# Kernel tuning notes

Measured on AMD Instinct MI355X. Metric: run time of the kernel, lower is better.

The kernel has to match this reference:

```python
import jax, jax.numpy as jnp
import numpy as np

IN_C, OUT_C, HEADS = 128, 64, 2
N_USER, N_ITEM, E = 100000, 50000, 500000
NEG_SLOPE = 0.2


def _params(key, in_c, out_c, heads):
    ks = jax.random.split(key, 4)
    s_lin = 1.0 / np.sqrt(in_c)
    s_att = 1.0 / np.sqrt(out_c)
    return dict(
        Wl=jax.random.normal(ks[0], (in_c, heads * out_c), jnp.float32) * s_lin,
        bl=jnp.zeros((heads * out_c,), jnp.float32),
        Wr=jax.random.normal(ks[1], (in_c, heads * out_c), jnp.float32) * s_lin,
        br=jnp.zeros((heads * out_c,), jnp.float32),
        att=jax.random.normal(ks[2], (heads, out_c), jnp.float32) * s_att,
        bias=jnp.zeros((out_c,), jnp.float32),
    )


def setup_inputs() -> dict:
    key = jax.random.key(0)
    k = jax.random.split(key, 8)
    inp = {
        "x_user": jax.random.normal(k[0], (N_USER, IN_C), jnp.float32),
        "x_item": jax.random.normal(k[1], (N_ITEM, IN_C), jnp.float32),
        "src_u2i": jax.random.randint(k[2], (E,), 0, N_USER, jnp.int32),
        "dst_u2i": jax.random.randint(k[3], (E,), 0, N_ITEM, jnp.int32),
        "src_i2u": jax.random.randint(k[4], (E,), 0, N_ITEM, jnp.int32),
        "dst_i2u": jax.random.randint(k[5], (E,), 0, N_USER, jnp.int32),
    }
    p_u2i = _params(k[6], IN_C, OUT_C, HEADS)
    p_i2u = _params(k[7], IN_C, OUT_C, HEADS)
    for n, v in p_u2i.items():
        inp[n + "_u2i"] = v
    for n, v in p_i2u.items():
        inp[n + "_i2u"] = v
    return inp


def gatv2_conv(x_src, x_dst, src, dst, Wl, bl, Wr, br, att, bias, n_dst):
    # lin_l on source nodes, lin_r on destination nodes -> [N, H, C]
    xl = (x_src @ Wl + bl).reshape(-1, HEADS, OUT_C)
    xr = (x_dst @ Wr + br).reshape(-1, HEADS, OUT_C)
    xj = xl[src]  # [E, H, C] gathered source features
    xi = xr[dst]  # [E, H, C] gathered dest features
    e = jax.nn.leaky_relu(xi + xj, NEG_SLOPE)
    logits = jnp.einsum("ehc,hc->eh", e, att)  # [E, H]
    # numerically stable segment softmax over incoming edges per dest node
    m = jax.ops.segment_max(logits, dst, num_segments=n_dst)
    m = jnp.where(jnp.isfinite(m), m, 0.0)  # guard empty segments
    a = jnp.exp(logits - m[dst])
    denom = jax.ops.segment_sum(a, dst, num_segments=n_dst)
    alpha = a / (denom[dst] + 1e-16)
    out = jax.ops.segment_sum(alpha[:, :, None] * xj, dst, num_segments=n_dst)
    return out.mean(axis=1) + bias  # concat=False -> head mean, then bias


def reference(x_user, x_item, src_u2i, dst_u2i, src_i2u, dst_i2u,
              Wl_u2i, bl_u2i, Wr_u2i, br_u2i, att_u2i, bias_u2i,
              Wl_i2u, bl_i2u, Wr_i2u, br_i2u, att_i2u, bias_i2u):
    # HeteroConv with aggr='sum': one edge type per destination node type here
    out_item = gatv2_conv(x_user, x_item, src_u2i, dst_u2i,
                          Wl_u2i, bl_u2i, Wr_u2i, br_u2i, att_u2i, bias_u2i, N_ITEM)
    out_user = gatv2_conv(x_item, x_user, src_i2u, dst_i2u,
                          Wl_i2u, bl_i2u, Wr_i2u, br_i2u, att_i2u, bias_i2u, N_USER)
    return out_user, out_item
```

## Files before the change

### kernel.cpp

```cpp
#include <hip/hip_runtime.h>

#define SCAN_B 1024

__global__ __launch_bounds__(256) void k_zero(int* __restrict__ cnt, int n) {
    int i = blockIdx.x * 256 + threadIdx.x;
    if (i < n) cnt[i] = 0;
}

__global__ __launch_bounds__(256) void k_hist(
    const int* __restrict__ dst_a, const int* __restrict__ dst_b,
    int* __restrict__ cnt, int n_a, int E)
{
    int i = blockIdx.x * 256 + threadIdx.x;
    if (i >= 2 * E) return;
    int idx = (i < E) ? dst_a[i] : (n_a + dst_b[i - E]);
    atomicAdd(&cnt[idx], 1);
}

__global__ __launch_bounds__(SCAN_B) void k_scan1(
    const int* __restrict__ cnt, int n, int* __restrict__ rowptr, int* __restrict__ bsum)
{
    __shared__ int tmp[SCAN_B];
    int i = blockIdx.x * SCAN_B + threadIdx.x;
    int v = (i < n) ? cnt[i] : 0;
    tmp[threadIdx.x] = v;
    __syncthreads();
    for (int off = 1; off < SCAN_B; off <<= 1) {
        int t = (threadIdx.x >= (unsigned)off) ? tmp[threadIdx.x - off] : 0;
        __syncthreads();
        tmp[threadIdx.x] += t;
        __syncthreads();
    }
    if (i < n) rowptr[i] = tmp[threadIdx.x] - v;
    if (threadIdx.x == SCAN_B - 1) bsum[blockIdx.x] = tmp[threadIdx.x];
}

__global__ __launch_bounds__(SCAN_B) void k_scan2(int* __restrict__ bsum, int nb) {
    __shared__ int tmp[SCAN_B];
    int i = threadIdx.x;
    int v = (i < nb) ? bsum[i] : 0;
    tmp[i] = v;
    __syncthreads();
    for (int off = 1; off < SCAN_B; off <<= 1) {
        int t = (i >= off) ? tmp[i - off] : 0;
        __syncthreads();
        tmp[i] += t;
        __syncthreads();
    }
    if (i < nb) bsum[i] = tmp[i] - v;
}

__global__ __launch_bounds__(256) void k_scan3(
    int* __restrict__ rowptr, int* __restrict__ cursor,
    const int* __restrict__ bsum, int n, int total)
{
    int i = blockIdx.x * 256 + threadIdx.x;
    if (i < n) {
        int r = rowptr[i] + bsum[i / SCAN_B];
        rowptr[i] = r;
        cursor[i] = r;
    }
    if (i == 0) rowptr[n] = total;
}

__global__ __launch_bounds__(256) void k_fill(
    const int* __restrict__ src_a, const int* __restrict__ dst_a,
    const int* __restrict__ src_b, const int* __restrict__ dst_b,
    int* __restrict__ cursor, int* __restrict__ sorted_src, int n_a, int E)
{
    int i = blockIdx.x * 256 + threadIdx.x;
    if (i >= 2 * E) return;
    int idx, s;
    if (i < E) { idx = dst_a[i];            s = src_a[i]; }
    else       { idx = n_a + dst_b[i - E];  s = src_b[i - E]; }
    int pos = atomicAdd(&cursor[idx], 1);
    sorted_src[pos] = s;
}

__global__ __launch_bounds__(256) void gemm128x2(
    const float* __restrict__ X0,
    const float* __restrict__ W00, const float* __restrict__ B00, float* __restrict__ Y00,
    const float* __restrict__ W01, const float* __restrict__ B01, float* __restrict__ Y01,
    int M0, int nb0,
    const float* __restrict__ X1,
    const float* __restrict__ W10, const float* __restrict__ B10, float* __restrict__ Y10,
    const float* __restrict__ W11, const float* __restrict__ B11, float* __restrict__ Y11,
    int M1)
{
    __shared__ float xs[64][20];
    __shared__ float ws[16][256];

    const float *X, *W0, *B0, *W1, *B1;
    float *Y0, *Y1;
    int M, bid;
    if ((int)blockIdx.x < nb0) {
        X = X0; W0 = W00; B0 = B00; Y0 = Y00; W1 = W01; B1 = B01; Y1 = Y01;
        M = M0; bid = blockIdx.x;
    } else {
        X = X1; W0 = W10; B0 = B10; Y0 = Y10; W1 = W11; B1 = B11; Y1 = Y11;
        M = M1; bid = blockIdx.x - nb0;
    }

    const int tid = threadIdx.x;
    const int m0  = bid * 64;
    const int r0  = (tid >> 4) * 4;
    const int c0  = (tid & 15) * 4;

    float acc[4][16];
#pragma unroll
    for (int i = 0; i < 4; ++i)
#pragma unroll
        for (int j = 0; j < 16; ++j) acc[i][j] = 0.0f;

    for (int kc = 0; kc < 128; kc += 16) {
        {
            int row = tid >> 2;
            int kq  = (tid & 3) * 4;
            float4 v = make_float4(0.f, 0.f, 0.f, 0.f);
            if (m0 + row < M)
                v = *(const float4*)&X[(size_t)(m0 + row) * 128 + kc + kq];
            *(float4*)&xs[row][kq] = v;
        }
#pragma unroll
        for (int i = 0; i < 4; ++i) {
            int f = tid + i * 256;
            int k = f >> 6;
            int q = (f & 63) * 4;
            float4 v = (q < 128)
                ? *(const float4*)&W0[(size_t)(kc + k) * 128 + q]
                : *(const float4*)&W1[(size_t)(kc + k) * 128 + (q - 128)];
            *(float4*)&ws[k][q] = v;
        }
        __syncthreads();

#pragma unroll
        for (int k = 0; k < 16; k += 4) {
            float4 a0 = *(const float4*)&xs[r0 + 0][k];
            float4 a1 = *(const float4*)&xs[r0 + 1][k];
            float4 a2 = *(const float4*)&xs[r0 + 2][k];
            float4 a3 = *(const float4*)&xs[r0 + 3][k];
#pragma unroll
            for (int kk = 0; kk < 4; ++kk) {
                float4 b0 = *(const float4*)&ws[k + kk][c0];
                float4 b1 = *(const float4*)&ws[k + kk][c0 + 64];
                float4 b2 = *(const float4*)&ws[k + kk][c0 + 128];
                float4 b3 = *(const float4*)&ws[k + kk][c0 + 192];
                float av[4] = { ((const float*)&a0)[kk], ((const float*)&a1)[kk],
                                ((const float*)&a2)[kk], ((const float*)&a3)[kk] };
#pragma unroll
                for (int i = 0; i < 4; ++i) {
                    float a = av[i];
                    acc[i][0]  += a * b0.x; acc[i][1]  += a * b0.y;
                    acc[i][2]  += a * b0.z; acc[i][3]  += a * b0.w;
                    acc[i][4]  += a * b1.x; acc[i][5]  += a * b1.y;
                    acc[i][6]  += a * b1.z; acc[i][7]  += a * b1.w;
                    acc[i][8]  += a * b2.x; acc[i][9]  += a * b2.y;
                    acc[i][10] += a * b2.z; acc[i][11] += a * b2.w;
                    acc[i][12] += a * b3.x; acc[i][13] += a * b3.y;
                    acc[i][14] += a * b3.z; acc[i][15] += a * b3.w;
                }
            }
        }
        __syncthreads();
    }

    float4 p00 = *(const float4*)&B0[c0];
    float4 p01 = *(const float4*)&B0[c0 + 64];
    float4 p10 = *(const float4*)&B1[c0];
    float4 p11 = *(const float4*)&B1[c0 + 64];
#pragma unroll
    for (int i = 0; i < 4; ++i) {
        int row = m0 + r0 + i;
        if (row < M) {
            *(float4*)&Y0[(size_t)row * 128 + c0] = make_float4(
                acc[i][0] + p00.x, acc[i][1] + p00.y, acc[i][2] + p00.z, acc[i][3] + p00.w);
            *(float4*)&Y0[(size_t)row * 128 + c0 + 64] = make_float4(
                acc[i][4] + p01.x, acc[i][5] + p01.y, acc[i][6] + p01.z, acc[i][7] + p01.w);
            *(float4*)&Y1[(size_t)row * 128 + c0] = make_float4(
                acc[i][8] + p10.x, acc[i][9] + p10.y, acc[i][10] + p10.z, acc[i][11] + p10.w);
            *(float4*)&Y1[(size_t)row * 128 + c0 + 64] = make_float4(
                acc[i][12] + p11.x, acc[i][13] + p11.y, acc[i][14] + p11.z, acc[i][15] + p11.w);
        }
    }
}

__global__ __launch_bounds__(256) void k_gat2(
    const float* __restrict__ xl_a, const float* __restrict__ xr_a,
    const float* __restrict__ att_a, const float* __restrict__ bias_a,
    float* __restrict__ out_a,
    const float* __restrict__ xl_b, const float* __restrict__ xr_b,
    const float* __restrict__ att_b, const float* __restrict__ bias_b,
    float* __restrict__ out_b,
    const int* __restrict__ rowptr, const int* __restrict__ srcs,
    int n_a, int n_all)
{
    int wave = (blockIdx.x * 256 + threadIdx.x) >> 6;
    if (wave >= n_all) return;
    const int lane = threadIdx.x & 63;
    const int h = lane >> 5;
    const int j = lane & 31;
    const int ch = h * 64 + 2 * j;

    const float *xl, *xr, *att, *bias;
    float* out;
    int d;
    if (wave < n_a) { xl = xl_a; xr = xr_a; att = att_a; bias = bias_a; out = out_a; d = wave; }
    else            { xl = xl_b; xr = xr_b; att = att_b; bias = bias_b; out = out_b; d = wave - n_a; }

    const int base = rowptr[wave];
    const int end  = rowptr[wave + 1];
    if (base == end) {
        if (lane < 32) {
            float2 bv = *(const float2*)&bias[2 * j];
            *(float2*)&out[(size_t)d * 64 + 2 * j] = bv;
        }
        return;
    }

    const float2 xi = *(const float2*)&xr[(size_t)d * 128 + ch];
    const float2 at = *(const float2*)&att[ch];

    float den = 0.f, a0 = 0.f, a1 = 0.f;
    int k = base;
    for (; k + 1 < end; k += 2) {
        int s0 = srcs[k];
        int s1 = srcs[k + 1];
        float2 x0 = *(const float2*)&xl[(size_t)s0 * 128 + ch];
        float2 x1 = *(const float2*)&xl[(size_t)s1 * 128 + ch];
        float e00 = xi.x + x0.x, e01 = xi.y + x0.y;
        float e10 = xi.x + x1.x, e11 = xi.y + x1.y;
        e00 = fmaxf(e00, 0.2f * e00);
        e01 = fmaxf(e01, 0.2f * e01);
        e10 = fmaxf(e10, 0.2f * e10);
        e11 = fmaxf(e11, 0.2f * e11);
        float p0 = e00 * at.x + e01 * at.y;
        float p1 = e10 * at.x + e11 * at.y;
        p0 += __shfl_xor(p0, 1, 64);  p1 += __shfl_xor(p1, 1, 64);
        p0 += __shfl_xor(p0, 2, 64);  p1 += __shfl_xor(p1, 2, 64);
        p0 += __shfl_xor(p0, 4, 64);  p1 += __shfl_xor(p1, 4, 64);
        p0 += __shfl_xor(p0, 8, 64);  p1 += __shfl_xor(p1, 8, 64);
        p0 += __shfl_xor(p0, 16, 64); p1 += __shfl_xor(p1, 16, 64);
        float w0 = __expf(p0);
        float w1 = __expf(p1);
        den += w0 + w1;
        a0  += w0 * x0.x + w1 * x1.x;
        a1  += w0 * x0.y + w1 * x1.y;
    }
    if (k < end) {
        int s0 = srcs[k];
        float2 x0 = *(const float2*)&xl[(size_t)s0 * 128 + ch];
        float e00 = xi.x + x0.x, e01 = xi.y + x0.y;
        e00 = fmaxf(e00, 0.2f * e00);
        e01 = fmaxf(e01, 0.2f * e01);
        float p0 = e00 * at.x + e01 * at.y;
        p0 += __shfl_xor(p0, 1, 64);
        p0 += __shfl_xor(p0, 2, 64);
        p0 += __shfl_xor(p0, 4, 64);
        p0 += __shfl_xor(p0, 8, 64);
        p0 += __shfl_xor(p0, 16, 64);
        float w0 = __expf(p0);
        den += w0;
        a0  += w0 * x0.x;
        a1  += w0 * x0.y;
    }

    float inv = 1.0f / (den + 1e-16f);
    float r0 = a0 * inv;
    float r1 = a1 * inv;
    float q0 = __shfl_xor(r0, 32, 64);
    float q1 = __shfl_xor(r1, 32, 64);
    if (lane < 32) {
        float2 bv = *(const float2*)&bias[2 * j];
        float2 o = make_float2(0.5f * (r0 + q0) + bv.x,
                               0.5f * (r1 + q1) + bv.y);
        *(float2*)&out[(size_t)d * 64 + 2 * j] = o;
    }
}

extern "C" void kernel_launch(void* const* d_in, const int* in_sizes, int n_in,
                              void* d_out, int out_size, void* d_ws, size_t ws_size,
                              hipStream_t stream)
{
    const float* x_user   = (const float*)d_in[0];
    const float* x_item   = (const float*)d_in[1];
    const int*   src_u2i  = (const int*)d_in[2];
    const int*   dst_u2i  = (const int*)d_in[3];
    const int*   src_i2u  = (const int*)d_in[4];
    const int*   dst_i2u  = (const int*)d_in[5];
    const float* Wl_u2i   = (const float*)d_in[6];
    const float* bl_u2i   = (const float*)d_in[7];
    const float* Wr_u2i   = (const float*)d_in[8];
    const float* br_u2i   = (const float*)d_in[9];
    const float* att_u2i  = (const float*)d_in[10];
    const float* bias_u2i = (const float*)d_in[11];
    const float* Wl_i2u   = (const float*)d_in[12];
    const float* bl_i2u   = (const float*)d_in[13];
    const float* Wr_i2u   = (const float*)d_in[14];
    const float* br_i2u   = (const float*)d_in[15];
    const float* att_i2u  = (const float*)d_in[16];
    const float* bias_i2u = (const float*)d_in[17];

    const int n_user = in_sizes[0] / 128;
    const int n_item = in_sizes[1] / 128;
    const int E      = in_sizes[2];
    const int n_all  = n_item + n_user;

    float* out_user = (float*)d_out;
    float* out_item = out_user + (size_t)n_user * 64;

    char* w = (char*)d_ws;
    float* xl_u2i = (float*)w; w += (size_t)n_user * 128 * 4;
    float* xr_u2i = (float*)w; w += (size_t)n_item * 128 * 4;
    float* xl_i2u = (float*)w; w += (size_t)n_item * 128 * 4;
    float* xr_i2u = (float*)w; w += (size_t)n_user * 128 * 4;
    int* srcs_all   = (int*)w; w += (size_t)2 * E * 4;
    int* rowptr_all = (int*)w; w += (size_t)(n_all + 1) * 4;
    int* cnt_all    = (int*)w; w += (size_t)n_all * 4;
    int* bsum       = (int*)w; w += (size_t)SCAN_B * 4;

    const int nb = (n_all + SCAN_B - 1) / SCAN_B;

    k_zero<<<(n_all + 255) / 256, 256, 0, stream>>>(cnt_all, n_all);
    k_hist<<<(2 * E + 255) / 256, 256, 0, stream>>>(dst_u2i, dst_i2u, cnt_all, n_item, E);
    k_scan1<<<nb, SCAN_B, 0, stream>>>(cnt_all, n_all, rowptr_all, bsum);
    k_scan2<<<1, SCAN_B, 0, stream>>>(bsum, nb);
    k_scan3<<<(n_all + 255) / 256, 256, 0, stream>>>(rowptr_all, cnt_all, bsum, n_all, 2 * E);
    k_fill<<<(2 * E + 255) / 256, 256, 0, stream>>>(
        src_u2i, dst_u2i, src_i2u, dst_i2u, cnt_all, srcs_all, n_item, E);

    const int nb_user = (n_user + 63) / 64;
    const int nb_item = (n_item + 63) / 64;
    gemm128x2<<<nb_user + nb_item, 256, 0, stream>>>(
        x_user, Wl_u2i, bl_u2i, xl_u2i, Wr_i2u, br_i2u, xr_i2u, n_user, nb_user,
        x_item, Wl_i2u, bl_i2u, xl_i2u, Wr_u2i, br_u2i, xr_u2i, n_item);

    k_gat2<<<(n_all + 3) / 4, 256, 0, stream>>>(
        xl_u2i, xr_u2i, att_u2i, bias_u2i, out_item,
        xl_i2u, xr_i2u, att_i2u, bias_i2u, out_user,
        rowptr_all, srcs_all, n_item, n_all);
}
```

Baseline: 448.7 us.

## Replace FP32 SIMT GEMM with split-bf16 MFMA GEMM using pre-transposed weights

Replaces the shared-memory FP32 FMA GEMM that projects node features with a per-wave MFMA kernel (16x16x32 bf16). Both operands are split into high and low bf16 parts, and three MFMAs per tile recover near-FP32 accuracy. A new prep kernel transposes and splits the weights into bf16 hi/lo buffers in the workspace. The cost is triple the MFMA work, an extra kernel launch, and weights read straight from global or L2 with no LDS staging. The epilogue also writes outputs as scalar strided stores instead of float4.

```diff
diff --git a/kernel.cpp b/kernel.cpp
--- a/kernel.cpp
+++ b/kernel.cpp
@@ -1,6 +1,30 @@
 #include <hip/hip_runtime.h>
 
 #define SCAN_B 1024
+
+typedef __attribute__((ext_vector_type(8))) short bf16x8;
+typedef __attribute__((ext_vector_type(4))) float f32x4;
+
+#define MFMA16(a, b, c) __builtin_amdgcn_mfma_f32_16x16x32_bf16(a, b, c, 0, 0, 0)
+
+__device__ __forceinline__ unsigned short bf16rn(float f) {
+    unsigned u = __float_as_uint(f);
+    u += 0x7fffu + ((u >> 16) & 1u);
+    return (unsigned short)(u >> 16);
+}
+
+__device__ __forceinline__ void packhl(const float4 v0, const float4 v1,
+                                       bf16x8* hi, bf16x8* lo)
+{
+    float e[8] = { v0.x, v0.y, v0.z, v0.w, v1.x, v1.y, v1.z, v1.w };
+#pragma unroll
+    for (int i = 0; i < 8; ++i) {
+        unsigned short h = bf16rn(e[i]);
+        (*hi)[i] = (short)h;
+        float hf = __uint_as_float((unsigned)h << 16);
+        (*lo)[i] = (short)bf16rn(e[i] - hf);
+    }
+}
 
 __global__ __launch_bounds__(256) void k_zero(int* __restrict__ cnt, int n) {
     int i = blockIdx.x * 256 + threadIdx.x;
@@ -77,109 +101,106 @@
     sorted_src[pos] = s;
 }
 
-__global__ __launch_bounds__(256) void gemm128x2(
+__global__ __launch_bounds__(64) void k_wprep(
+    const float* __restrict__ W0u, const float* __restrict__ W1u,
+    const float* __restrict__ W0i, const float* __restrict__ W1i,
+    unsigned short* __restrict__ WTuh, unsigned short* __restrict__ WTul,
+    unsigned short* __restrict__ WTih, unsigned short* __restrict__ WTil)
+{
+    int b = blockIdx.x;
+    int dir = b >> 8;
+    int n = b & 255;
+    const float* W = (n < 128) ? (dir ? W0i : W0u) : (dir ? W1i : W1u);
+    unsigned short* Th = dir ? WTih : WTuh;
+    unsigned short* Tl = dir ? WTil : WTul;
+    int col = n & 127;
+    for (int k = threadIdx.x; k < 128; k += 64) {
+        float w = W[(size_t)k * 128 + col];
+        unsigned short h = bf16rn(w);
+        float hf = __uint_as_float((unsigned)h << 16);
+        unsigned short l = bf16rn(w - hf);
+        Th[(size_t)n * 128 + k] = h;
+        Tl[(size_t)n * 128 + k] = l;
+    }
+}
+
+__global__ __launch_bounds__(256) void gemm_mfma(
     const float* __restrict__ X0,
-    const float* __restrict__ W00, const float* __restrict__ B00, float* __restrict__ Y00,
-    const float* __restrict__ W01, const float* __restrict__ B01, float* __restrict__ Y01,
-    int M0, int nb0,
+    const unsigned short* __restrict__ WT0h, const unsigned short* __restrict__ WT0l,
+    const float* __restrict__ B00, const float* __restrict__ B01,
+    float* __restrict__ Y00, float* __restrict__ Y01, int M0, int nw0,
     const float* __restrict__ X1,
-    const float* __restrict__ W10, const float* __restrict__ B10, float* __restrict__ Y10,
-    const float* __restrict__ W11, const float* __restrict__ B11, float* __restrict__ Y11,
-    int M1)
-{
-    __shared__ float xs[64][20];
-    __shared__ float ws[16][256];
-
-    const float *X, *W0, *B0, *W1, *B1;
-    float *Y0, *Y1;
-    int M, bid;
-    if ((int)blockIdx.x < nb0) {
-        X = X0; W0 = W00; B0 = B00; Y0 = Y00; W1 = W01; B1 = B01; Y1 = Y01;
-        M = M0; bid = blockIdx.x;
-    } else {
-        X = X1; W0 = W10; B0 = B10; Y0 = Y10; W1 = W11; B1 = B11; Y1 = Y11;
-        M = M1; bid = blockIdx.x - nb0;
-    }
-
-    const int tid = threadIdx.x;
-    const int m0  = bid * 64;
-    const int r0  = (tid >> 4) * 4;
-    const int c0  = (tid & 15) * 4;
-
-    float acc[4][16];
-#pragma unroll
-    for (int i = 0; i < 4; ++i)
-#pragma unroll
-        for (int j = 0; j < 16; ++j) acc[i][j] = 0.0f;
-
-    for (int kc = 0; kc < 128; kc += 16) {
-        {
-            int row = tid >> 2;
-            int kq  = (tid & 3) * 4;
-            float4 v = make_float4(0.f, 0.f, 0.f, 0.f);
-            if (m0 + row < M)
-                v = *(const float4*)&X[(size_t)(m0 + row) * 128 + kc + kq];
-            *(float4*)&xs[row][kq] = v;
+    const unsigned short* __restrict__ WT1h, const unsigned short* __restrict__ WT1l,
+    const float* __restrict__ B10, const float* __restrict__ B11,
+    float* __restrict__ Y10, float* __restrict__ Y11, int M1, int nw_all)
+{
+    int gw = (blockIdx.x * 256 + threadIdx.x) >> 6;
+    if (gw >= nw_all) return;
+    const int lane = threadIdx.x & 63;
+
+    const float* X; const unsigned short *Wh, *Wl; const float *B0, *B1;
+    float *Y0, *Y1; int M, strip;
+    if (gw < nw0) { X = X0; Wh = WT0h; Wl = WT0l; B0 = B00; B1 = B01;
+                    Y0 = Y00; Y1 = Y01; M = M0; strip = gw; }
+    else          { X = X1; Wh = WT1h; Wl = WT1l; B0 = B10; B1 = B11;
+                    Y0 = Y10; Y1 = Y11; M = M1; strip = gw - nw0; }
+
+    const int r0   = strip * 32;
+    const int cw   = lane & 15;
+    const int g    = lane >> 4;
+    const int rA   = r0 + cw;
+    const int rB   = rA + 16;
+    const bool vA  = rA < M;
+    const bool vB  = rB < M;
+    const float* xpA = X + (size_t)rA * 128;
+    const float* xpB = X + (size_t)rB * 128;
+    const unsigned short* wph = Wh + (size_t)cw * 128;
+    const unsigned short* wpl = Wl + (size_t)cw * 128;
+
+    f32x4 acc0[16], acc1[16];
+#pragma unroll
+    for (int j = 0; j < 16; ++j) {
+        acc0[j] = (f32x4){0.f, 0.f, 0.f, 0.f};
+        acc1[j] = (f32x4){0.f, 0.f, 0.f, 0.f};
+    }
+
+    const float4 z4 = make_float4(0.f, 0.f, 0.f, 0.f);
+#pragma unroll
+    for (int kc = 0; kc < 128; kc += 32) {
+        const int kb = kc + g * 8;
+        float4 a0 = vA ? *(const float4*)(xpA + kb)     : z4;
+        float4 a1 = vA ? *(const float4*)(xpA + kb + 4) : z4;
+        float4 a2 = vB ? *(const float4*)(xpB + kb)     : z4;
+        float4 a3 = vB ? *(const float4*)(xpB + kb + 4) : z4;
+        bf16x8 ah0, al0, ah1, al1;
+        packhl(a0, a1, &ah0, &al0);
+        packhl(a2, a3, &ah1, &al1);
+#pragma unroll
+        for (int j = 0; j < 16; ++j) {
+            const size_t off = (size_t)j * 16 * 128 + kb;
+            bf16x8 bh = *(const bf16x8*)(wph + off);
+            bf16x8 bl = *(const bf16x8*)(wpl + off);
+            acc0[j] = MFMA16(ah0, bh, acc0[j]);
+            acc0[j] = MFMA16(al0, bh, acc0[j]);
+            acc0[j] = MFMA16(ah0, bl, acc0[j]);
+            acc1[j] = MFMA16(ah1, bh, acc1[j]);
+            acc1[j] = MFMA16(al1, bh, acc1[j]);
+            acc1[j] = MFMA16(ah1, bl, acc1[j]);
         }
-#pragma unroll
-        for (int i = 0; i < 4; ++i) {
-            int f = tid + i * 256;
-            int k = f >> 6;
-            int q = (f & 63) * 4;
-            float4 v = (q < 128)
-                ? *(const float4*)&W0[(size_t)(kc + k) * 128 + q]
-                : *(const float4*)&W1[(size_t)(kc + k) * 128 + (q - 128)];
-            *(float4*)&ws[k][q] = v;
-        }
-        __syncthreads();
-
-#pragma unroll
-        for (int k = 0; k < 16; k += 4) {
-            float4 a0 = *(const float4*)&xs[r0 + 0][k];
-            float4 a1 = *(const float4*)&xs[r0 + 1][k];
-            float4 a2 = *(const float4*)&xs[r0 + 2][k];
-            float4 a3 = *(const float4*)&xs[r0 + 3][k];
-#pragma unroll
-            for (int kk = 0; kk < 4; ++kk) {
-                float4 b0 = *(const float4*)&ws[k + kk][c0];
-                float4 b1 = *(const float4*)&ws[k + kk][c0 + 64];
-                float4 b2 = *(const float4*)&ws[k + kk][c0 + 128];
-                float4 b3 = *(const float4*)&ws[k + kk][c0 + 192];
-                float av[4] = { ((const float*)&a0)[kk], ((const float*)&a1)[kk],
-                                ((const float*)&a2)[kk], ((const float*)&a3)[kk] };
-#pragma unroll
-                for (int i = 0; i < 4; ++i) {
-                    float a = av[i];
-                    acc[i][0]  += a * b0.x; acc[i][1]  += a * b0.y;
-                    acc[i][2]  += a * b0.z; acc[i][3]  += a * b0.w;
-                    acc[i][4]  += a * b1.x; acc[i][5]  += a * b1.y;
-                    acc[i][6]  += a * b1.z; acc[i][7]  += a * b1.w;
-                    acc[i][8]  += a * b2.x; acc[i][9]  += a * b2.y;
-                    acc[i][10] += a * b2.z; acc[i][11] += a * b2.w;
-                    acc[i][12] += a * b3.x; acc[i][13] += a * b3.y;
-                    acc[i][14] += a * b3.z; acc[i][15] += a * b3.w;
-                }
-            }
-        }
-        __syncthreads();
-    }
-
-    float4 p00 = *(const float4*)&B0[c0];
-    float4 p01 = *(const float4*)&B0[c0 + 64];
-    float4 p10 = *(const float4*)&B1[c0];
-    float4 p11 = *(const float4*)&B1[c0 + 64];
-#pragma unroll
-    for (int i = 0; i < 4; ++i) {
-        int row = m0 + r0 + i;
-        if (row < M) {
-            *(float4*)&Y0[(size_t)row * 128 + c0] = make_float4(
-                acc[i][0] + p00.x, acc[i][1] + p00.y, acc[i][2] + p00.z, acc[i][3] + p00.w);
-            *(float4*)&Y0[(size_t)row * 128 + c0 + 64] = make_float4(
-                acc[i][4] + p01.x, acc[i][5] + p01.y, acc[i][6] + p01.z, acc[i][7] + p01.w);
-            *(float4*)&Y1[(size_t)row * 128 + c0] = make_float4(
-                acc[i][8] + p10.x, acc[i][9] + p10.y, acc[i][10] + p10.z, acc[i][11] + p10.w);
-            *(float4*)&Y1[(size_t)row * 128 + c0 + 64] = make_float4(
-                acc[i][12] + p11.x, acc[i][13] + p11.y, acc[i][14] + p11.z, acc[i][15] + p11.w);
+    }
+
+    const int rs = r0 + g * 4;
+#pragma unroll
+    for (int j = 0; j < 16; ++j) {
+        float* Yt = (j < 8) ? Y0 : Y1;
+        const float* Bt = (j < 8) ? B0 : B1;
+        int cc = ((j & 7) * 16) + cw;
+        float bv = Bt[cc];
+#pragma unroll
+        for (int r = 0; r < 4; ++r) {
+            int R = rs + r;
+            if (R < M)      Yt[(size_t)R * 128 + cc]        = acc0[j][r] + bv;
+            if (R + 16 < M) Yt[(size_t)(R + 16) * 128 + cc] = acc1[j][r] + bv;
         }
     }
 }
@@ -317,8 +338,15 @@
     int* rowptr_all = (int*)w; w += (size_t)(n_all + 1) * 4;
     int* cnt_all    = (int*)w; w += (size_t)n_all * 4;
     int* bsum       = (int*)w; w += (size_t)SCAN_B * 4;
+    unsigned short* WTuh = (unsigned short*)w; w += (size_t)256 * 128 * 2;
+    unsigned short* WTul = (unsigned short*)w; w += (size_t)256 * 128 * 2;
+    unsigned short* WTih = (unsigned short*)w; w += (size_t)256 * 128 * 2;
+    unsigned short* WTil = (unsigned short*)w; w += (size_t)256 * 128 * 2;
 
     const int nb = (n_all + SCAN_B - 1) / SCAN_B;
+
+    k_wprep<<<512, 64, 0, stream>>>(Wl_u2i, Wr_i2u, Wl_i2u, Wr_u2i,
+                                    WTuh, WTul, WTih, WTil);
 
     k_zero<<<(n_all + 255) / 256, 256, 0, stream>>>(cnt_all, n_all);
     k_hist<<<(2 * E + 255) / 256, 256, 0, stream>>>(dst_u2i, dst_i2u, cnt_all, n_item, E);
@@ -328,11 +356,12 @@
     k_fill<<<(2 * E + 255) / 256, 256, 0, stream>>>(
         src_u2i, dst_u2i, src_i2u, dst_i2u, cnt_all, srcs_all, n_item, E);
 
-    const int nb_user = (n_user + 63) / 64;
-    const int nb_item = (n_item + 63) / 64;
-    gemm128x2<<<nb_user + nb_item, 256, 0, stream>>>(
-        x_user, Wl_u2i, bl_u2i, xl_u2i, Wr_i2u, br_i2u, xr_i2u, n_user, nb_user,
-        x_item, Wl_i2u, bl_i2u, xl_i2u, Wr_u2i, br_u2i, xr_u2i, n_item);
+    const int nw0 = (n_user + 31) / 32;
+    const int nw1 = (n_item + 31) / 32;
+    const int nw_all = nw0 + nw1;
+    gemm_mfma<<<(nw_all + 3) / 4, 256, 0, stream>>>(
+        x_user, WTuh, WTul, bl_u2i, br_i2u, xl_u2i, xr_i2u, n_user, nw0,
+        x_item, WTih, WTil, bl_i2u, br_u2i, xl_i2u, xr_u2i, n_item, nw_all);
 
     k_gat2<<<(n_all + 3) / 4, 256, 0, stream>>>(
         xl_u2i, xr_u2i, att_u2i, bias_u2i, out_item,
```

Measured after the change: 538.5 us. 20.0% more time.
